# Kernel optimization log

Hardware: AMD Instinct MI355X
Metric: run time of the kernel (lower is better)

Reference implementation:

```python
import jax, jax.numpy as jnp
import numpy as np

D_IN, D, SEQ, B = 512, 1024, 2048, 8
EPS = 1e-5


def positional_encoding(seq_len, d):
    pos = np.arange(seq_len)[:, None].astype(np.float32)
    i = np.arange(d)[None, :].astype(np.float32)
    angle_rads = pos / (10000.0 ** (2.0 * np.floor(i / 2.0) / np.float32(d)))
    angle_rads[:, 0::2] = np.sin(angle_rads[:, 0::2])
    angle_rads[:, 1::2] = np.cos(angle_rads[:, 1::2])
    return jnp.asarray(angle_rads[None, ...], dtype=jnp.float32)  # [1, s, d]


def setup_inputs() -> dict:
    key = jax.random.key(0)
    ks = jax.random.split(key, 10)
    def lin(k, fan_in, shape):
        bound = 1.0 / np.sqrt(fan_in)
        return jax.random.uniform(k, shape, jnp.float32, -bound, bound)
    return {
        "inputs": jax.random.normal(ks[0], (B, SEQ, D_IN), jnp.float32),
        "embed_w": lin(ks[1], D_IN, (D, D_IN)),
        "embed_b": lin(ks[2], D_IN, (D,)),
        "wq_w": lin(ks[3], D, (D, D)), "wq_b": lin(ks[3], D, (D,)),
        "wk_w": lin(ks[4], D, (D, D)), "wk_b": lin(ks[4], D, (D,)),
        "wv_w": lin(ks[5], D, (D, D)), "wv_b": lin(ks[5], D, (D,)),
        "ln_g": jnp.ones((D,), jnp.float32),
        "ln_b": jnp.zeros((D,), jnp.float32),
        "soft_key_w": lin(ks[6], D, (D, D)),
        "soft_query": jax.random.normal(ks[7], (D,), jnp.float32),
        "pos_enc": positional_encoding(SEQ, D),
    }


def reference(inputs, embed_w, embed_b, wq_w, wq_b, wk_w, wk_b, wv_w, wv_b,
              ln_g, ln_b, soft_key_w, soft_query, pos_enc):
    x = jnp.einsum('bsi,oi->bso', inputs, embed_w) + embed_b  # embed
    x = x + pos_enc  # broadcast positional encoding over batch
    Q = jnp.einsum('bsd,od->bso', x, wq_w) + wq_b
    K = jnp.einsum('bsd,od->bso', x, wk_w) + wk_b
    V = jnp.einsum('bsd,od->bso', x, wv_w) + wv_b
    score = jnp.einsum('bso,bio->bsi', Q, K) / jnp.sqrt(jnp.float32(D))
    score = jax.nn.softmax(score, axis=2)
    Z = jnp.einsum('bsi,bio->bso', score, V)
    h = x + Z
    mu = jnp.mean(h, axis=-1, keepdims=True)
    var = jnp.mean(jnp.square(h - mu), axis=-1, keepdims=True)
    H = (h - mu) * jax.lax.rsqrt(var + EPS) * ln_g + ln_b
    soft_key = jnp.tanh(jnp.einsum('bsd,od->bso', H, soft_key_w))
    soft_score = jax.nn.softmax(jnp.einsum('bso,o->bs', soft_key, soft_query), axis=1)
    return jnp.einsum('bs,bso->bo', soft_score, H)
```

## Files before the change

### kernel.cpp

```cpp
#include <hip/hip_runtime.h>
#include <hip/hip_bf16.h>
#include <math.h>

typedef __bf16 bf16_t;
typedef bf16_t bf16x8 __attribute__((ext_vector_type(8)));
typedef bf16_t bf16x4 __attribute__((ext_vector_type(4)));
typedef float  f32x4  __attribute__((ext_vector_type(4)));

#define D_IN   512
#define DMODEL 1024
#define SEQ    2048
#define BATCH  8
#define NTOK   (BATCH*SEQ)

typedef __attribute__((address_space(1))) unsigned int gu32;
typedef __attribute__((address_space(3))) unsigned int lu32;

__device__ __forceinline__ void async16(const void* g, void* l) {
    __builtin_amdgcn_global_load_lds((gu32*)g, (lu32*)l, 16, 0, 0);
}

template<int EPI>
__global__ __launch_bounds__(256)
void gemm_bt(const bf16_t* __restrict__ Ab, const bf16_t* __restrict__ Bb,
             bf16_t* __restrict__ Cb, int K, int ldc, int gx, int gy,
             long batchA, long batchB, long batchC,
             const float* __restrict__ bias, const float* __restrict__ aux_f,
             const bf16_t* __restrict__ resid, float* __restrict__ logits,
             const float* __restrict__ bias3)
{
    constexpr int SMEM_ELEMS = (EPI == 4) ? 32768 : 16384;
    __shared__ __align__(16) bf16_t smem[SMEM_ELEMS];
    bf16_t* As = smem;
    bf16_t* Bs = smem + 8192;

    const int tid  = threadIdx.x;
    const int lane = tid & 63;
    const int wave = tid >> 6;

    const int flat = blockIdx.x;
    const int nb   = gridDim.x;
    const int vid  = (flat & 7) * (nb >> 3) + (flat >> 3);
    const int pb   = gx * gy;
    const int z    = vid / pb;
    const int w    = vid - z * pb;
    const int sy   = w / (gx * 4);
    const int r    = w - sy * (gx * 4);
    const int sx   = r >> 4;
    const int inner= r & 15;
    const int mtile = (sy * 4 + (inner & 3)) * 128;
    const int ntile = (sx * 4 + (inner >> 2)) * 128;

    const bf16_t* A  = Ab + (long)z * batchA;
    const bf16_t* Bp = Bb + (long)z * batchB;

    f32x4 acc[4][4];
    #pragma unroll
    for (int i = 0; i < 4; ++i)
        #pragma unroll
        for (int j = 0; j < 4; ++j)
            acc[i][j] = (f32x4)(0.f);

    const int lr  = lane & 15;
    const int lr7 = lr & 7;
    const int lq  = lane >> 4;

    const int wrow = (wave >> 1) * 64;
    const int wcol = (wave & 1) * 64;

    const int srow8 = lane >> 3;
    const int sk    = ((lane & 7) ^ srow8) * 8;

    for (int k0 = 0; k0 < K; k0 += 64) {
        __syncthreads();
        #pragma unroll
        for (int j = 0; j < 4; ++j) {
            const int g   = (wave << 2) + j;
            const int row = (g << 3) + srow8;
            async16(A  + (long)(mtile + row) * K + (k0 + sk), &As[g << 9]);
            async16(Bp + (long)(ntile + row) * K + (k0 + sk), &Bs[g << 9]);
        }
        __syncthreads();

        #pragma unroll
        for (int s = 0; s < 2; ++s) {
            const int po = ((lq + (s << 2)) ^ lr7) << 3;
            bf16x8 af[4], bf[4];
            #pragma unroll
            for (int t = 0; t < 4; ++t)
                af[t] = *(const bf16x8*)&As[(wrow + t*16 + lr)*64 + po];
            #pragma unroll
            for (int t = 0; t < 4; ++t)
                bf[t] = *(const bf16x8*)&Bs[(wcol + t*16 + lr)*64 + po];
            #pragma unroll
            for (int tr = 0; tr < 4; ++tr)
                #pragma unroll
                for (int tc = 0; tc < 4; ++tc)
                    acc[tr][tc] = __builtin_amdgcn_mfma_f32_16x16x32_bf16(
                                      af[tr], bf[tc], acc[tr][tc], 0, 0, 0);
        }
    }

    if constexpr (EPI == 5) {
        const int mbase = mtile + wrow + lq*4;
        #pragma unroll
        for (int tr = 0; tr < 4; ++tr) {
            #pragma unroll
            for (int reg = 0; reg < 4; ++reg) {
                const int m = mbase + tr*16 + reg;
                float rs = 0.f;
                #pragma unroll
                for (int tc = 0; tc < 4; ++tc) {
                    const int n = ntile + wcol + tc*16 + lr;
                    rs += tanhf(acc[tr][tc][reg]) * aux_f[n];
                }
                rs += __shfl_xor(rs, 1);
                rs += __shfl_xor(rs, 2);
                rs += __shfl_xor(rs, 4);
                rs += __shfl_xor(rs, 8);
                if (lr == 0) atomicAdd(&logits[m], rs);
            }
        }
        return;
    }

    __syncthreads();

    if constexpr (EPI == 4) {
        float* fsm = (float*)smem;
        #pragma unroll
        for (int tr = 0; tr < 4; ++tr) {
            #pragma unroll
            for (int reg = 0; reg < 4; ++reg) {
                const int rl = wrow + tr*16 + lq*4 + reg;
                #pragma unroll
                for (int tc = 0; tc < 4; ++tc) {
                    const int cl = wcol + tc*16 + lr;
                    fsm[rl*128 + ((((cl >> 2) ^ (rl & 31)) << 2) | (cl & 3))] = acc[tr][tc][reg];
                }
            }
        }
        __syncthreads();
        bf16_t* C = Cb + (long)z * batchC;
        const int chunk = tid & 15;
        const int grp   = tid >> 4;
        #pragma unroll
        for (int rep = 0; rep < 8; ++rep) {
            const int R  = grp + rep*16;
            const int c0 = chunk*8;
            const int p0 = (((c0 >> 2)       ^ (R & 31)) << 2);
            const int p1 = ((((c0 + 4) >> 2) ^ (R & 31)) << 2);
            const f32x4 f0 = *(const f32x4*)&fsm[R*128 + p0];
            const f32x4 f1 = *(const f32x4*)&fsm[R*128 + p1];
            const long off = (long)(mtile + R)*ldc + ntile + c0;
            const bf16x8 r8 = *(const bf16x8*)&resid[(long)z*batchC + off];
            bf16x8 val;
            #pragma unroll
            for (int i = 0; i < 4; ++i) {
                val[i]     = (bf16_t)(f0[i] + (float)r8[i]);
                val[i + 4] = (bf16_t)(f1[i] + (float)r8[i + 4]);
            }
            *(bf16x8*)&C[off] = val;
        }
        return;
    }

    const int seg = (EPI == 6) ? (ntile >> 10) : 0;
    const float* bp = bias;
    if constexpr (EPI == 6) bp = (seg == 0) ? bias : (seg == 1) ? aux_f : bias3;

    #pragma unroll
    for (int tr = 0; tr < 4; ++tr) {
        #pragma unroll
        for (int reg = 0; reg < 4; ++reg) {
            const int rl = wrow + tr*16 + lq*4 + reg;
            #pragma unroll
            for (int tc = 0; tc < 4; ++tc) {
                const int cl = wcol + tc*16 + lr;
                float v = acc[tr][tc][reg];
                if constexpr (EPI == 0)
                    v += bias[ntile + cl] + aux_f[((mtile + rl) & (SEQ-1))*DMODEL + ntile + cl];
                if constexpr (EPI == 3) v *= 0.03125f;
                if constexpr (EPI == 6) v += bp[(ntile + cl) & 1023];
                smem[rl*128 + ((((cl >> 3) ^ (rl & 7)) << 3) | (cl & 7))] = (bf16_t)v;
            }
        }
    }
    __syncthreads();

    if constexpr (EPI == 6) {
        if (seg == 2) {
            bf16_t* VTb = Cb + 33554432;
            const int col  = tid & 127;
            const int half = tid >> 7;
            const int b    = mtile >> 11, s0 = mtile & (SEQ-1);
            const long nbase = (long)b*DMODEL + (ntile & 1023) + col;
            #pragma unroll
            for (int rep = 0; rep < 8; ++rep) {
                const int R0 = half*64 + rep*8;
                bf16x8 o;
                #pragma unroll
                for (int i = 0; i < 8; ++i) {
                    const int rl = R0 + i;
                    o[i] = smem[rl*128 + ((((col >> 3) ^ (rl & 7)) << 3) | (col & 7))];
                }
                *(bf16x8*)&VTb[nbase*SEQ + s0 + R0] = o;
            }
            return;
        }
        const int chunk = tid & 15;
        const int grp   = tid >> 4;
        const long base = (long)seg * 16777216 + (ntile & 1023) + chunk*8;
        #pragma unroll
        for (int rep = 0; rep < 8; ++rep) {
            const int R = grp + rep*16;
            const int phys = chunk ^ (R & 7);
            bf16x8 val = *(const bf16x8*)&smem[R*128 + phys*8];
            *(bf16x8*)&Cb[base + (long)(mtile + R)*1024] = val;
        }
        return;
    }

    bf16_t* C = Cb + (long)z * batchC;
    const int chunk = tid & 15;
    const int grp   = tid >> 4;
    #pragma unroll
    for (int rep = 0; rep < 8; ++rep) {
        const int R = grp + rep*16;
        const int phys = chunk ^ (R & 7);
        bf16x8 val = *(const bf16x8*)&smem[R*128 + phys*8];
        const long off = (long)(mtile + R)*ldc + ntile + chunk*8;
        *(bf16x8*)&C[off] = val;
    }
}

__global__ void cast_f32_bf16(const float* __restrict__ s, bf16_t* __restrict__ d, int n4) {
    int i = blockIdx.x*256 + threadIdx.x;
    if (i < n4) {
        const float4 f = ((const float4*)s)[i];
        bf16x4 o;
        o.x = (bf16_t)f.x; o.y = (bf16_t)f.y; o.z = (bf16_t)f.z; o.w = (bf16_t)f.w;
        ((bf16x4*)d)[i] = o;
    }
}

__global__ void zero_f32_k(float* __restrict__ p, int n) {
    int i = blockIdx.x*256 + threadIdx.x;
    if (i < n) p[i] = 0.f;
}

__global__ __launch_bounds__(256) void softmax_rows_bf16(bf16_t* __restrict__ P) {
    bf16_t* row = P + (long)blockIdx.x * SEQ;
    const int t = threadIdx.x, lane = t & 63, wave = t >> 6;
    __shared__ float sm[8];
    float v[8]; float mx = -3.0e38f;
    #pragma unroll
    for (int j = 0; j < 8; ++j) { v[j] = (float)row[t + 256*j]; mx = fmaxf(mx, v[j]); }
    #pragma unroll
    for (int o = 32; o; o >>= 1) mx = fmaxf(mx, __shfl_xor(mx, o));
    if (lane == 0) sm[wave] = mx;
    __syncthreads();
    mx = fmaxf(fmaxf(sm[0], sm[1]), fmaxf(sm[2], sm[3]));
    float s = 0.f;
    #pragma unroll
    for (int j = 0; j < 8; ++j) { v[j] = __expf(v[j] - mx); s += v[j]; }
    #pragma unroll
    for (int o = 32; o; o >>= 1) s += __shfl_xor(s, o);
    if (lane == 0) sm[4 + wave] = s;
    __syncthreads();
    s = (sm[4] + sm[5]) + (sm[6] + sm[7]);
    const float inv = 1.f / s;
    #pragma unroll
    for (int j = 0; j < 8; ++j) row[t + 256*j] = (bf16_t)(v[j] * inv);
}

__global__ __launch_bounds__(256) void softmax_vec(const float* __restrict__ L, float* __restrict__ W) {
    const float* l = L + (long)blockIdx.x * SEQ;
    float* w = W + (long)blockIdx.x * SEQ;
    const int t = threadIdx.x, lane = t & 63, wave = t >> 6;
    __shared__ float sm[8];
    float v[8]; float mx = -3.0e38f;
    #pragma unroll
    for (int j = 0; j < 8; ++j) { v[j] = l[t + 256*j]; mx = fmaxf(mx, v[j]); }
    #pragma unroll
    for (int o = 32; o; o >>= 1) mx = fmaxf(mx, __shfl_xor(mx, o));
    if (lane == 0) sm[wave] = mx;
    __syncthreads();
    mx = fmaxf(fmaxf(sm[0], sm[1]), fmaxf(sm[2], sm[3]));
    float s = 0.f;
    #pragma unroll
    for (int j = 0; j < 8; ++j) { v[j] = __expf(v[j] - mx); s += v[j]; }
    #pragma unroll
    for (int o = 32; o; o >>= 1) s += __shfl_xor(s, o);
    if (lane == 0) sm[4 + wave] = s;
    __syncthreads();
    s = (sm[4] + sm[5]) + (sm[6] + sm[7]);
    const float inv = 1.f / s;
    #pragma unroll
    for (int j = 0; j < 8; ++j) w[t + 256*j] = v[j] * inv;
}

__global__ __launch_bounds__(256) void layernorm_k(const bf16_t* __restrict__ h, bf16_t* __restrict__ H,
                                                   const float* __restrict__ gam, const float* __restrict__ bet) {
    const long row = blockIdx.x;
    const bf16_t* hr = h + row*DMODEL;
    bf16_t* Hr = H + row*DMODEL;
    const int t = threadIdx.x, lane = t & 63, wave = t >> 6;
    __shared__ float sm[8];
    float v[4]; float s = 0.f, q = 0.f;
    #pragma unroll
    for (int j = 0; j < 4; ++j) { v[j] = (float)hr[t + 256*j]; s += v[j]; q += v[j]*v[j]; }
    #pragma unroll
    for (int o = 32; o; o >>= 1) { s += __shfl_xor(s, o); q += __shfl_xor(q, o); }
    if (lane == 0) { sm[wave] = s; sm[4 + wave] = q; }
    __syncthreads();
    s = (sm[0] + sm[1]) + (sm[2] + sm[3]);
    q = (sm[4] + sm[5]) + (sm[6] + sm[7]);
    const float mu  = s * (1.f/DMODEL);
    const float var = q * (1.f/DMODEL) - mu*mu;
    const float r   = rsqrtf(var + 1e-5f);
    #pragma unroll
    for (int j = 0; j < 4; ++j) {
        const int n = t + 256*j;
        Hr[n] = (bf16_t)((v[j] - mu)*r*gam[n] + bet[n]);
    }
}

__global__ __launch_bounds__(256) void pool_partial(const float* __restrict__ w,
                                                    const bf16_t* __restrict__ H,
                                                    float* __restrict__ part) {
    const int b = blockIdx.y;
    const int c = blockIdx.x;
    const int t = threadIdx.x;
    const bf16_t* Hb = H + ((long)b*SEQ + (long)c*32)*DMODEL;
    const float*  wb = w + b*SEQ + c*32;
    f32x4 s = (f32x4)(0.f);
    #pragma unroll 4
    for (int i = 0; i < 32; ++i) {
        const float wi = wb[i];
        const bf16x4 hv = *(const bf16x4*)&Hb[(long)i*DMODEL + t*4];
        s[0] += wi * (float)hv[0];
        s[1] += wi * (float)hv[1];
        s[2] += wi * (float)hv[2];
        s[3] += wi * (float)hv[3];
    }
    *(f32x4*)&part[((long)b*64 + c)*DMODEL + t*4] = s;
}

__global__ __launch_bounds__(256) void pool_reduce(const float* __restrict__ part,
                                                   float* __restrict__ out) {
    const int i = blockIdx.x*256 + threadIdx.x;
    const int b = i >> 10, o = i & 1023;
    const float* p = part + (long)b*64*DMODEL + o;
    float s = 0.f;
    #pragma unroll
    for (int c = 0; c < 64; ++c) s += p[c*DMODEL];
    out[i] = s;
}

extern "C" void kernel_launch(void* const* d_in, const int* in_sizes, int n_in,
                              void* d_out, int out_size, void* d_ws, size_t ws_size,
                              hipStream_t stream) {
    (void)in_sizes; (void)n_in; (void)out_size; (void)ws_size;
    const float* inp = (const float*)d_in[0];
    const float* emw = (const float*)d_in[1];
    const float* emb = (const float*)d_in[2];
    const float* wqw = (const float*)d_in[3];
    const float* wqb = (const float*)d_in[4];
    const float* wkw = (const float*)d_in[5];
    const float* wkb = (const float*)d_in[6];
    const float* wvw = (const float*)d_in[7];
    const float* wvb = (const float*)d_in[8];
    const float* lng = (const float*)d_in[9];
    const float* lnb = (const float*)d_in[10];
    const float* skw = (const float*)d_in[11];
    const float* sq  = (const float*)d_in[12];
    const float* pos = (const float*)d_in[13];
    float* out = (float*)d_out;

    char* ws = (char*)d_ws;
    bf16_t* in_b   = (bf16_t*)(ws + 0);
    bf16_t* we_b   = (bf16_t*)(ws + 16777216);
    bf16_t* wq_b   = (bf16_t*)(ws + 17825792);
    bf16_t* wk_b   = (bf16_t*)(ws + 19922944);
    bf16_t* wv_b   = (bf16_t*)(ws + 22020096);
    bf16_t* sk_b   = (bf16_t*)(ws + 24117248);
    float*  logits = (float*)(ws + 26214400);
    float*  wsoft  = (float*)(ws + 26279936);
    bf16_t* xb     = (bf16_t*)(ws + 26345472);
    bf16_t* Qb     = (bf16_t*)(ws + 59899904);
    bf16_t* Kb     = (bf16_t*)(ws + 93454336);
    bf16_t* VT     = (bf16_t*)(ws + 127008768);
    bf16_t* Hb     = (bf16_t*)(ws + 160563200);
    bf16_t* Pb     = (bf16_t*)(ws + 194117632);
    float*  part   = (float*)(ws + 0);

    cast_f32_bf16<<<8192, 256, 0, stream>>>(inp, in_b, 2097152);
    cast_f32_bf16<<<512,  256, 0, stream>>>(emw, we_b, 131072);
    cast_f32_bf16<<<1024, 256, 0, stream>>>(wqw, wq_b, 262144);
    cast_f32_bf16<<<1024, 256, 0, stream>>>(wkw, wk_b, 262144);
    cast_f32_bf16<<<1024, 256, 0, stream>>>(wvw, wv_b, 262144);
    cast_f32_bf16<<<1024, 256, 0, stream>>>(skw, sk_b, 262144);
    zero_f32_k<<<64, 256, 0, stream>>>(logits, NTOK);

    gemm_bt<0><<<1024, 256, 0, stream>>>(in_b, we_b, xb, D_IN, DMODEL, 8, 128,
        0, 0, 0, emb, pos, nullptr, nullptr, nullptr);
    gemm_bt<6><<<3072, 256, 0, stream>>>(xb, wq_b, Qb, DMODEL, DMODEL, 24, 128,
        0, 0, 0, wqb, wkb, nullptr, nullptr, wvb);
    gemm_bt<3><<<2048, 256, 0, stream>>>(Qb, Kb, Pb, DMODEL, SEQ, 16, 16,
        (long)SEQ*DMODEL, (long)SEQ*DMODEL, (long)SEQ*SEQ, nullptr, nullptr, nullptr, nullptr, nullptr);
    softmax_rows_bf16<<<NTOK, 256, 0, stream>>>(Pb);
    gemm_bt<4><<<1024, 256, 0, stream>>>(Pb, VT, Qb, SEQ, DMODEL, 8, 16,
        (long)SEQ*SEQ, (long)DMODEL*SEQ, (long)SEQ*DMODEL, nullptr, nullptr, xb, nullptr, nullptr);
    layernorm_k<<<NTOK, 256, 0, stream>>>(Qb, Hb, lng, lnb);
    gemm_bt<5><<<1024, 256, 0, stream>>>(Hb, sk_b, nullptr, DMODEL, 0, 8, 128,
        0, 0, 0, nullptr, sq, nullptr, logits, nullptr);
    softmax_vec<<<BATCH, 256, 0, stream>>>(logits, wsoft);
    pool_partial<<<dim3(64, BATCH), 256, 0, stream>>>(wsoft, Hb, part);
    pool_reduce<<<32, 256, 0, stream>>>(part, out);
}
```

Before: 552.4 us.

## Double-buffer LDS tiles in the bf16 GEMM to overlap loads with MFMA

The GEMM main loop now ping-pongs between two LDS buffers. While the current K-slice is being computed with MFMA, the next slice's global-to-LDS async loads are already in flight, so each iteration needs only one barrier instead of load-then-wait serialization. This doubles shared memory per block to 64 KB for every epilogue variant, which may lower occupancy, and it relies on the barrier draining outstanding async loads.

Result: faster. 519.1 us (-6.0%).

```diff
diff --git a/kernel.cpp b/kernel.cpp
--- a/kernel.cpp
+++ b/kernel.cpp
@@ -29,10 +29,7 @@
              const bf16_t* __restrict__ resid, float* __restrict__ logits,
              const float* __restrict__ bias3)
 {
-    constexpr int SMEM_ELEMS = (EPI == 4) ? 32768 : 16384;
-    __shared__ __align__(16) bf16_t smem[SMEM_ELEMS];
-    bf16_t* As = smem;
-    bf16_t* Bs = smem + 8192;
+    __shared__ __align__(16) bf16_t smem[32768];
 
     const int tid  = threadIdx.x;
     const int lane = tid & 63;
@@ -71,27 +68,45 @@
     const int srow8 = lane >> 3;
     const int sk    = ((lane & 7) ^ srow8) * 8;
 
-    for (int k0 = 0; k0 < K; k0 += 64) {
-        __syncthreads();
+    {
+        bf16_t* Ad = smem;
+        bf16_t* Bd = smem + 8192;
         #pragma unroll
         for (int j = 0; j < 4; ++j) {
             const int g   = (wave << 2) + j;
             const int row = (g << 3) + srow8;
-            async16(A  + (long)(mtile + row) * K + (k0 + sk), &As[g << 9]);
-            async16(Bp + (long)(ntile + row) * K + (k0 + sk), &Bs[g << 9]);
-        }
+            async16(A  + (long)(mtile + row) * K + sk, &Ad[g << 9]);
+            async16(Bp + (long)(ntile + row) * K + sk, &Bd[g << 9]);
+        }
+    }
+
+    int cur = 0;
+    for (int k0 = 0; k0 < K; k0 += 64) {
         __syncthreads();
-
+        if (k0 + 64 < K) {
+            bf16_t* Ad = smem + ((cur ^ 1) << 14);
+            bf16_t* Bd = Ad + 8192;
+            const int kn = k0 + 64;
+            #pragma unroll
+            for (int j = 0; j < 4; ++j) {
+                const int g   = (wave << 2) + j;
+                const int row = (g << 3) + srow8;
+                async16(A  + (long)(mtile + row) * K + (kn + sk), &Ad[g << 9]);
+                async16(Bp + (long)(ntile + row) * K + (kn + sk), &Bd[g << 9]);
+            }
+        }
+        const bf16_t* Ar = smem + (cur << 14);
+        const bf16_t* Br = Ar + 8192;
         #pragma unroll
         for (int s = 0; s < 2; ++s) {
             const int po = ((lq + (s << 2)) ^ lr7) << 3;
             bf16x8 af[4], bf[4];
             #pragma unroll
             for (int t = 0; t < 4; ++t)
-                af[t] = *(const bf16x8*)&As[(wrow + t*16 + lr)*64 + po];
+                af[t] = *(const bf16x8*)&Ar[(wrow + t*16 + lr)*64 + po];
             #pragma unroll
             for (int t = 0; t < 4; ++t)
-                bf[t] = *(const bf16x8*)&Bs[(wcol + t*16 + lr)*64 + po];
+                bf[t] = *(const bf16x8*)&Br[(wcol + t*16 + lr)*64 + po];
             #pragma unroll
             for (int tr = 0; tr < 4; ++tr)
                 #pragma unroll
@@ -99,6 +114,7 @@
                     acc[tr][tc] = __builtin_amdgcn_mfma_f32_16x16x32_bf16(
                                       af[tr], bf[tc], acc[tr][tc], 0, 0, 0);
         }
+        cur ^= 1;
     }
 
     if constexpr (EPI == 5) {
```

## Warp-specialize GEMM with a producer wave and 4-stage LDS ring

Applied to the files above, without the earlier changes.

Adds a fifth wave per block that acts as a dedicated async loader, filling a 4-deep ring of 32-wide K tiles in LDS. The four compute waves spin on volatile LDS flags instead of block-wide barriers. This is meant to overlap global-to-LDS loads with MFMA work and remove the per-step __syncthreads stalls. The cost is spin-wait overhead, all GEMM variants now using the full 64KB of shared memory (lower occupancy), halved K per step, and the risk of races in the hand-rolled flag protocol.

Result: slower. 931.7 us (+68.7%).

```diff
diff --git a/kernel.cpp b/kernel.cpp
--- a/kernel.cpp
+++ b/kernel.cpp
@@ -21,7 +21,7 @@
 }
 
 template<int EPI>
-__global__ __launch_bounds__(256)
+__global__ __launch_bounds__(320)
 void gemm_bt(const bf16_t* __restrict__ Ab, const bf16_t* __restrict__ Bb,
              bf16_t* __restrict__ Cb, int K, int ldc, int gx, int gy,
              long batchA, long batchB, long batchC,
@@ -29,10 +29,8 @@
              const bf16_t* __restrict__ resid, float* __restrict__ logits,
              const float* __restrict__ bias3)
 {
-    constexpr int SMEM_ELEMS = (EPI == 4) ? 32768 : 16384;
-    __shared__ __align__(16) bf16_t smem[SMEM_ELEMS];
-    bf16_t* As = smem;
-    bf16_t* Bs = smem + 8192;
+    __shared__ __align__(16) bf16_t smem[32768];
+    __shared__ int flags[8];
 
     const int tid  = threadIdx.x;
     const int lane = tid & 63;
@@ -54,6 +52,12 @@
     const bf16_t* A  = Ab + (long)z * batchA;
     const bf16_t* Bp = Bb + (long)z * batchB;
 
+    const int NT = K >> 5;
+
+    if (tid == 0) { flags[0] = 0; flags[4] = 0; flags[5] = 0; flags[6] = 0; flags[7] = 0; }
+    __syncthreads();
+    volatile int* vf = flags;
+
     f32x4 acc[4][4];
     #pragma unroll
     for (int i = 0; i < 4; ++i)
@@ -62,36 +66,54 @@
             acc[i][j] = (f32x4)(0.f);
 
     const int lr  = lane & 15;
-    const int lr7 = lr & 7;
     const int lq  = lane >> 4;
-
     const int wrow = (wave >> 1) * 64;
     const int wcol = (wave & 1) * 64;
 
-    const int srow8 = lane >> 3;
-    const int sk    = ((lane & 7) ^ srow8) * 8;
-
-    for (int k0 = 0; k0 < K; k0 += 64) {
-        __syncthreads();
-        #pragma unroll
-        for (int j = 0; j < 4; ++j) {
-            const int g   = (wave << 2) + j;
-            const int row = (g << 3) + srow8;
-            async16(A  + (long)(mtile + row) * K + (k0 + sk), &As[g << 9]);
-            async16(Bp + (long)(ntile + row) * K + (k0 + sk), &Bs[g << 9]);
-        }
-        __syncthreads();
-
-        #pragma unroll
-        for (int s = 0; s < 2; ++s) {
-            const int po = ((lq + (s << 2)) ^ lr7) << 3;
+    if (wave == 4) {
+        const int srow = lane >> 2;
+        const int skq  = (((lane & 3) ^ ((srow >> 1) & 3)) << 3);
+        auto stage = [&](int t) {
+            bf16_t* As_t = smem + ((t & 3) << 13);
+            bf16_t* Bs_t = As_t + 4096;
+            const long kk = (t << 5) + skq;
+            #pragma unroll
+            for (int j = 0; j < 8; ++j) {
+                const int row = (j << 4) + srow;
+                async16(A  + (long)(mtile + row) * K + kk, &As_t[j << 9]);
+                async16(Bp + (long)(ntile + row) * K + kk, &Bs_t[j << 9]);
+            }
+        };
+        stage(0);
+        stage(1);
+        for (int t = 0; t < NT; ++t) {
+            if (t + 1 < NT) asm volatile("s_waitcnt vmcnt(16)" ::: "memory");
+            else            asm volatile("s_waitcnt vmcnt(0)"  ::: "memory");
+            if (lane == 0) vf[0] = t + 1;
+            if (t + 2 < NT) {
+                const int need = t - 1;
+                while (vf[4] < need || vf[5] < need || vf[6] < need || vf[7] < need)
+                    __builtin_amdgcn_s_sleep(1);
+                asm volatile("" ::: "memory");
+                stage(t + 2);
+            }
+        }
+    } else {
+        const int po = (lq ^ ((lr >> 1) & 3)) << 3;
+        for (int t = 0; t < NT; ++t) {
+            while (vf[0] < t + 1) __builtin_amdgcn_s_sleep(1);
+            asm volatile("" ::: "memory");
+            const bf16_t* Ar = smem + ((t & 3) << 13);
+            const bf16_t* Br = Ar + 4096;
             bf16x8 af[4], bf[4];
             #pragma unroll
-            for (int t = 0; t < 4; ++t)
-                af[t] = *(const bf16x8*)&As[(wrow + t*16 + lr)*64 + po];
-            #pragma unroll
-            for (int t = 0; t < 4; ++t)
-                bf[t] = *(const bf16x8*)&Bs[(wcol + t*16 + lr)*64 + po];
+            for (int i = 0; i < 4; ++i)
+                af[i] = *(const bf16x8*)&Ar[(wrow + i*16 + lr)*32 + po];
+            #pragma unroll
+            for (int i = 0; i < 4; ++i)
+                bf[i] = *(const bf16x8*)&Br[(wcol + i*16 + lr)*32 + po];
+            asm volatile("s_waitcnt lgkmcnt(0)" ::: "memory");
+            if (lane == 0) vf[4 + wave] = t + 1;
             #pragma unroll
             for (int tr = 0; tr < 4; ++tr)
                 #pragma unroll
@@ -102,23 +124,25 @@
     }
 
     if constexpr (EPI == 5) {
-        const int mbase = mtile + wrow + lq*4;
-        #pragma unroll
-        for (int tr = 0; tr < 4; ++tr) {
-            #pragma unroll
-            for (int reg = 0; reg < 4; ++reg) {
-                const int m = mbase + tr*16 + reg;
-                float rs = 0.f;
-                #pragma unroll
-                for (int tc = 0; tc < 4; ++tc) {
-                    const int n = ntile + wcol + tc*16 + lr;
-                    rs += tanhf(acc[tr][tc][reg]) * aux_f[n];
+        if (wave < 4) {
+            const int mbase = mtile + wrow + lq*4;
+            #pragma unroll
+            for (int tr = 0; tr < 4; ++tr) {
+                #pragma unroll
+                for (int reg = 0; reg < 4; ++reg) {
+                    const int m = mbase + tr*16 + reg;
+                    float rs = 0.f;
+                    #pragma unroll
+                    for (int tc = 0; tc < 4; ++tc) {
+                        const int n = ntile + wcol + tc*16 + lr;
+                        rs += tanhf(acc[tr][tc][reg]) * aux_f[n];
+                    }
+                    rs += __shfl_xor(rs, 1);
+                    rs += __shfl_xor(rs, 2);
+                    rs += __shfl_xor(rs, 4);
+                    rs += __shfl_xor(rs, 8);
+                    if (lr == 0) atomicAdd(&logits[m], rs);
                 }
-                rs += __shfl_xor(rs, 1);
-                rs += __shfl_xor(rs, 2);
-                rs += __shfl_xor(rs, 4);
-                rs += __shfl_xor(rs, 8);
-                if (lr == 0) atomicAdd(&logits[m], rs);
             }
         }
         return;
@@ -128,39 +152,43 @@
 
     if constexpr (EPI == 4) {
         float* fsm = (float*)smem;
-        #pragma unroll
-        for (int tr = 0; tr < 4; ++tr) {
-            #pragma unroll
-            for (int reg = 0; reg < 4; ++reg) {
-                const int rl = wrow + tr*16 + lq*4 + reg;
-                #pragma unroll
-                for (int tc = 0; tc < 4; ++tc) {
-                    const int cl = wcol + tc*16 + lr;
-                    fsm[rl*128 + ((((cl >> 2) ^ (rl & 31)) << 2) | (cl & 3))] = acc[tr][tc][reg];
+        if (tid < 256) {
+            #pragma unroll
+            for (int tr = 0; tr < 4; ++tr) {
+                #pragma unroll
+                for (int reg = 0; reg < 4; ++reg) {
+                    const int rl = wrow + tr*16 + lq*4 + reg;
+                    #pragma unroll
+                    for (int tc = 0; tc < 4; ++tc) {
+                        const int cl = wcol + tc*16 + lr;
+                        fsm[rl*128 + ((((cl >> 2) ^ (rl & 31)) << 2) | (cl & 3))] = acc[tr][tc][reg];
+                    }
                 }
             }
         }
         __syncthreads();
-        bf16_t* C = Cb + (long)z * batchC;
-        const int chunk = tid & 15;
-        const int grp   = tid >> 4;
-        #pragma unroll
-        for (int rep = 0; rep < 8; ++rep) {
-            const int R  = grp + rep*16;
-            const int c0 = chunk*8;
-            const int p0 = (((c0 >> 2)       ^ (R & 31)) << 2);
-            const int p1 = ((((c0 + 4) >> 2) ^ (R & 31)) << 2);
-            const f32x4 f0 = *(const f32x4*)&fsm[R*128 + p0];
-            const f32x4 f1 = *(const f32x4*)&fsm[R*128 + p1];
-            const long off = (long)(mtile + R)*ldc + ntile + c0;
-            const bf16x8 r8 = *(const bf16x8*)&resid[(long)z*batchC + off];
-            bf16x8 val;
-            #pragma unroll
-            for (int i = 0; i < 4; ++i) {
-                val[i]     = (bf16_t)(f0[i] + (float)r8[i]);
-                val[i + 4] = (bf16_t)(f1[i] + (float)r8[i + 4]);
-            }
-            *(bf16x8*)&C[off] = val;
+        if (tid < 256) {
+            bf16_t* C = Cb + (long)z * batchC;
+            const int chunk = tid & 15;
+            const int grp   = tid >> 4;
+            #pragma unroll
+            for (int rep = 0; rep < 8; ++rep) {
+                const int R  = grp + rep*16;
+                const int c0 = chunk*8;
+                const int p0 = (((c0 >> 2)       ^ (R & 31)) << 2);
+                const int p1 = ((((c0 + 4) >> 2) ^ (R & 31)) << 2);
+                const f32x4 f0 = *(const f32x4*)&fsm[R*128 + p0];
+                const f32x4 f1 = *(const f32x4*)&fsm[R*128 + p1];
+                const long off = (long)(mtile + R)*ldc + ntile + c0;
+                const bf16x8 r8 = *(const bf16x8*)&resid[(long)z*batchC + off];
+                bf16x8 val;
+                #pragma unroll
+                for (int i = 0; i < 4; ++i) {
+                    val[i]     = (bf16_t)(f0[i] + (float)r8[i]);
+                    val[i + 4] = (bf16_t)(f1[i] + (float)r8[i + 4]);
+                }
+                *(bf16x8*)&C[off] = val;
+            }
         }
         return;
     }
@@ -169,24 +197,27 @@
     const float* bp = bias;
     if constexpr (EPI == 6) bp = (seg == 0) ? bias : (seg == 1) ? aux_f : bias3;
 
-    #pragma unroll
-    for (int tr = 0; tr < 4; ++tr) {
+    if (tid < 256) {
         #pragma unroll
-        for (int reg = 0; reg < 4; ++reg) {
-            const int rl = wrow + tr*16 + lq*4 + reg;
-            #pragma unroll
-            for (int tc = 0; tc < 4; ++tc) {
-                const int cl = wcol + tc*16 + lr;
-                float v = acc[tr][tc][reg];
-                if constexpr (EPI == 0)
-                    v += bias[ntile + cl] + aux_f[((mtile + rl) & (SEQ-1))*DMODEL + ntile + cl];
-                if constexpr (EPI == 3) v *= 0.03125f;
-                if constexpr (EPI == 6) v += bp[(ntile + cl) & 1023];
-                smem[rl*128 + ((((cl >> 3) ^ (rl & 7)) << 3) | (cl & 7))] = (bf16_t)v;
-            }
-        }
-    }
-    __syncthreads();
+        for (int tr = 0; tr < 4; ++tr) {
+            #pragma unroll
+            for (int reg = 0; reg < 4; ++reg) {
+                const int rl = wrow + tr*16 + lq*4 + reg;
+                #pragma unroll
+                for (int tc = 0; tc < 4; ++tc) {
+                    const int cl = wcol + tc*16 + lr;
+                    float v = acc[tr][tc][reg];
+                    if constexpr (EPI == 0)
+                        v += bias[ntile + cl] + aux_f[((mtile + rl) & (SEQ-1))*DMODEL + ntile + cl];
+                    if constexpr (EPI == 3) v *= 0.03125f;
+                    if constexpr (EPI == 6) v += bp[(ntile + cl) & 1023];
+                    smem[rl*128 + ((((cl >> 3) ^ (rl & 7)) << 3) | (cl & 7))] = (bf16_t)v;
+                }
+            }
+        }
+    }
+    __syncthreads();
+    if (tid >= 256) return;
 
     if constexpr (EPI == 6) {
         if (seg == 2) {
@@ -403,17 +434,17 @@
     cast_f32_bf16<<<1024, 256, 0, stream>>>(skw, sk_b, 262144);
     zero_f32_k<<<64, 256, 0, stream>>>(logits, NTOK);
 
-    gemm_bt<0><<<1024, 256, 0, stream>>>(in_b, we_b, xb, D_IN, DMODEL, 8, 128,
+    gemm_bt<0><<<1024, 320, 0, stream>>>(in_b, we_b, xb, D_IN, DMODEL, 8, 128,
         0, 0, 0, emb, pos, nullptr, nullptr, nullptr);
-    gemm_bt<6><<<3072, 256, 0, stream>>>(xb, wq_b, Qb, DMODEL, DMODEL, 24, 128,
+    gemm_bt<6><<<3072, 320, 0, stream>>>(xb, wq_b, Qb, DMODEL, DMODEL, 24, 128,
         0, 0, 0, wqb, wkb, nullptr, nullptr, wvb);
-    gemm_bt<3><<<2048, 256, 0, stream>>>(Qb, Kb, Pb, DMODEL, SEQ, 16, 16,
+    gemm_bt<3><<<2048, 320, 0, stream>>>(Qb, Kb, Pb, DMODEL, SEQ, 16, 16,
         (long)SEQ*DMODEL, (long)SEQ*DMODEL, (long)SEQ*SEQ, nullptr, nullptr, nullptr, nullptr, nullptr);
     softmax_rows_bf16<<<NTOK, 256, 0, stream>>>(Pb);
-    gemm_bt<4><<<1024, 256, 0, stream>>>(Pb, VT, Qb, SEQ, DMODEL, 8, 16,
+    gemm_bt<4><<<1024, 320, 0, stream>>>(Pb, VT, Qb, SEQ, DMODEL, 8, 16,
         (long)SEQ*SEQ, (long)DMODEL*SEQ, (long)SEQ*DMODEL, nullptr, nullptr, xb, nullptr, nullptr);
     layernorm_k<<<NTOK, 256, 0, stream>>>(Qb, Hb, lng, lnb);
-    gemm_bt<5><<<1024, 256, 0, stream>>>(Hb, sk_b, nullptr, DMODEL, 0, 8, 128,
+    gemm_bt<5><<<1024, 320, 0, stream>>>(Hb, sk_b, nullptr, DMODEL, 0, 8, 128,
         0, 0, 0, nullptr, sq, nullptr, logits, nullptr);
     softmax_vec<<<BATCH, 256, 0, stream>>>(logits, wsoft);
     pool_partial<<<dim3(64, BATCH), 256, 0, stream>>>(wsoft, Hb, part);
```
